# Kernel optimization log

Measured on AMD Instinct MI355X. Metric: run time of the kernel, lower is better.

The kernel has to match this reference:

```python
import jax, jax.numpy as jnp
import numpy as np

B, CIN, COUT, RES, K, WDIM = 16, 512, 512, 64, 3, 512


def setup_inputs() -> dict:
    key = jax.random.key(0)
    ks = jax.random.split(key, 6)
    return {
        "x": jax.random.normal(ks[0], (B, CIN, RES, RES), jnp.float32),
        "w": jax.random.normal(ks[1], (B, WDIM), jnp.float32),
        "affine_w": jax.random.normal(ks[2], (3 * CIN, WDIM), jnp.float32),
        "affine_b": jnp.ones((3 * CIN,), jnp.float32),  # bias_init=1
        "weight": jax.random.normal(ks[3], (COUT, CIN, K, K), jnp.float32),
        "bias": jnp.zeros((COUT,), jnp.float32),
        "noise_const": jax.random.normal(ks[4], (RES, RES), jnp.float32),
        "noise_strength": jnp.zeros((), jnp.float32),
    }


def reference(x, w, affine_w, affine_b, weight, bias, noise_const, noise_strength):
    b, cin, h, wd = x.shape
    cout, _, kh, kw = weight.shape
    wdim = affine_w.shape[1]
    # StyleSplit: FullyConnectedLayer (weight_gain = 1/sqrt(w_dim)) -> chunk3 -> m1*m2+m3
    proj = w @ (affine_w * (1.0 / np.sqrt(wdim))).T + affine_b  # [B, 3*Cin]
    m1, m2, m3 = jnp.split(proj, 3, axis=1)
    styles = m1 * m2 + m3  # [B, Cin]
    # modulate + demodulate (fused_modconv path)
    ww = weight[None] * styles[:, None, :, None, None]  # [B, Cout, Cin, kh, kw]
    dcoefs = jax.lax.rsqrt(jnp.sum(ww * ww, axis=(2, 3, 4)) + 1e-8)  # [B, Cout]
    ww = ww * dcoefs[:, :, None, None, None]
    # batch-as-groups conv (flip_weight=True -> plain cross-correlation), padding = k//2
    pad = kh // 2
    xg = x.reshape(1, b * cin, h, wd)
    wg = ww.reshape(b * cout, cin, kh, kw)
    y = jax.lax.conv_general_dilated(
        xg, wg, window_strides=(1, 1), padding=((pad, pad), (pad, pad)),
        dimension_numbers=("NCHW", "OIHW", "NCHW"), feature_group_count=b)
    y = y.reshape(b, cout, h, wd)
    # const noise
    y = y + noise_const * noise_strength
    # bias_act: lrelu(slope 0.2) with def_gain sqrt(2), gain=1, no clamp
    y = jax.nn.leaky_relu(y + bias[None, :, None, None], 0.2) * np.sqrt(2.0).astype(np.float32)
    return y
```

## Files before the change

kernel.cpp:

```cpp
#include <hip/hip_runtime.h>


#define NCI  512
#define NCO  512

typedef __attribute__((ext_vector_type(8))) short short8;
typedef __attribute__((ext_vector_type(4))) float f32x4;

#define GLDS16(g, l) __builtin_amdgcn_global_load_lds( \
    (const __attribute__((address_space(1))) void*)(g), \
    (__attribute__((address_space(3))) void*)(l), 16, 0, 0)

static __device__ __forceinline__ unsigned short f2bf(float f) {
  unsigned int u = __float_as_uint(f);
  u += 0x7fffu + ((u >> 16) & 1u);
  return (unsigned short)(u >> 16);
}

__global__ __launch_bounds__(256) void k_styles(
    const float* __restrict__ w, const float* __restrict__ aw,
    const float* __restrict__ ab, float* __restrict__ styles) {
  const int ci0 = blockIdx.x * 32, b = blockIdx.y;
  __shared__ float ws[512];
  __shared__ float pm[3][32];
  const int t = threadIdx.x;
  ws[t] = w[b * 512 + t];
  ws[t + 256] = w[b * 512 + 256 + t];
  __syncthreads();
  const int r = t >> 3, k = t & 7;
#pragma unroll
  for (int pass = 0; pass < 3; ++pass) {
    const float* row = aw + (size_t)(ci0 + r + pass * 512) * 512;
    float a = 0.f;
#pragma unroll 4
    for (int i = 0; i < 16; ++i) {
      float4 v = *(const float4*)(row + i * 32 + k * 4);
      float4 u = *(const float4*)(&ws[i * 32 + k * 4]);
      a += v.x * u.x + v.y * u.y + v.z * u.z + v.w * u.w;
    }
    a += __shfl_xor(a, 1); a += __shfl_xor(a, 2); a += __shfl_xor(a, 4);
    if (k == 0) pm[pass][r] = a;
  }
  __syncthreads();
  if (t < 32) {
    const float g = 0.04419417382415922f;
    int j = ci0 + t;
    float m1 = pm[0][t] * g + ab[j];
    float m2 = pm[1][t] * g + ab[j + 512];
    float m3 = pm[2][t] * g + ab[j + 1024];
    styles[b * 512 + j] = m1 * m2 + m3;
  }
}

__global__ __launch_bounds__(256) void k_wt(
    const float* __restrict__ wgt, short* __restrict__ wb2, float* __restrict__ wsq) {
  const int t = blockIdx.x * 256 + threadIdx.x;
  const int co = t >> 9, ci = t & 511;
  const float* p = wgt + (size_t)t * 9;
  const int ci_blk = ci >> 5, co_blk = co >> 6, m = (co >> 4) & 3;
  const int lane2 = ((ci >> 3) & 3) * 16 + (co & 15), e = ci & 7;
  const size_t base = (size_t)(ci_blk * 8 + co_blk) * 18432 + (size_t)m * 512 + lane2 * 8 + e;
  float s = 0.f;
#pragma unroll
  for (int kk = 0; kk < 9; ++kk) {
    float v = p[kk];
    s += v * v;
    wb2[base + (size_t)kk * 2048] = (short)f2bf(v);
  }
  wsq[t] = s;
}

__global__ __launch_bounds__(256) void k_dcoef(
    const float* __restrict__ wsq, const float* __restrict__ styles,
    float* __restrict__ dcoef) {
  const int co0 = blockIdx.x * 32, b = blockIdx.y;
  __shared__ float ss[512];
  const int t = threadIdx.x;
  float s0 = styles[b * 512 + t], s1 = styles[b * 512 + 256 + t];
  ss[t] = s0 * s0;
  ss[t + 256] = s1 * s1;
  __syncthreads();
  const int r = t >> 3, k = t & 7;
  const float* row = wsq + (size_t)(co0 + r) * 512;
  float a = 0.f;
#pragma unroll 4
  for (int i = 0; i < 16; ++i) {
    float4 v = *(const float4*)(row + i * 32 + k * 4);
    float4 u = *(const float4*)(&ss[i * 32 + k * 4]);
    a += v.x * u.x + v.y * u.y + v.z * u.z + v.w * u.w;
  }
  a += __shfl_xor(a, 1); a += __shfl_xor(a, 2); a += __shfl_xor(a, 4);
  if (k == 0) dcoef[b * 512 + co0 + r] = 1.0f / sqrtf(a + 1e-8f);
}

__global__ __launch_bounds__(256) void k_xt(
    const float* __restrict__ x, const float* __restrict__ styles,
    short* __restrict__ xt) {
  const int px0 = blockIdx.x * 64, ci0 = blockIdx.y * 32, b = blockIdx.z;
  __shared__ float tile[32][68];
  const int t = threadIdx.x;
  {
    const int cil = t >> 4, pxq = t & 15;
#pragma unroll
    for (int half = 0; half < 2; ++half) {
      const int c = cil + half * 16;
      float4 v = *(const float4*)(x + ((size_t)(b * 512 + ci0 + c)) * 4096 + px0 + pxq * 4);
      float sc = styles[b * 512 + ci0 + c];
      v.x *= sc; v.y *= sc; v.z *= sc; v.w *= sc;
      *(float4*)(&tile[c][pxq * 4]) = v;
    }
  }
  __syncthreads();
  {
    const int pxl = t >> 2, cig = t & 3;
    short8 o;
#pragma unroll
    for (int e = 0; e < 8; ++e) o[e] = (short)f2bf(tile[cig * 8 + e][pxl]);
    *(short8*)(xt + ((size_t)(b * 4096 + px0 + pxl)) * 512 + ci0 + cig * 8) = o;
  }
}

__global__ __launch_bounds__(256, 2) void k_conv(
    const short* __restrict__ xt, const short* __restrict__ wb2,
    const float* __restrict__ dcoef, const float* __restrict__ bias,
    const float* __restrict__ noise, const float* __restrict__ nstr,
    float* __restrict__ out) {
  const int bid = blockIdx.x;
  const int logical = (bid & 7) * 256 + (bid >> 3);
  const int co0 = (logical & 7) * 64;
  const int h0  = ((logical >> 3) & 15) * 4;
  const int b   = logical >> 7;

  __shared__ short xs2[6][4][66][8];
  __shared__ short wls2[9][4][64][8];
  const int t = threadIdx.x;
  const int lane = t & 63, wave = t >> 6;
  const int lrow = lane & 15, lq = lane >> 4;

  const short8 z8 = {0, 0, 0, 0, 0, 0, 0, 0};
  if (t < 48) {
    int r = t / 8, pc = t & 7;
    *(short8*)(&xs2[r][pc >> 1][(pc & 1) ? 65 : 0][0]) = z8;
  }
  if (h0 == 0)
    for (int i = t; i < 264; i += 256) ((short8*)&xs2[0][0][0][0])[i] = z8;
  if (h0 == 60)
    for (int i = t; i < 264; i += 256) ((short8*)&xs2[5][0][0][0])[i] = z8;

  f32x4 acc[4][4];
#pragma unroll
  for (int m = 0; m < 4; ++m)
#pragma unroll
    for (int n = 0; n < 4; ++n)
#pragma unroll
      for (int e = 0; e < 4; ++e) acc[m][n][e] = 0.f;

  const size_t xb = (size_t)b * 4096 * 512;
  const int cob = co0 >> 6;

  for (int cb = 0; cb < 16; ++cb) {
    const int ci0 = cb * 32;
#pragma unroll
    for (int i = 0; i < 6; ++i) {
      int rp = i * 4 + wave;
      int r = rp >> 2, p = rp & 3;
      int row = h0 - 1 + r;
      if ((unsigned)row < 64u) {
        const short* g = xt + xb + ((size_t)(row * 64 + lane)) * 512 + ci0 + p * 8;
        GLDS16(g, &xs2[r][p][1][0]);
      }
    }
    const short* wbase = wb2 + (size_t)(cb * 8 + cob) * 18432;
#pragma unroll
    for (int i = 0; i < 9; ++i) {
      int c = i * 4 + wave;
      GLDS16(wbase + c * 512 + lane * 8, ((short*)wls2) + c * 512);
    }
    __syncthreads();

#pragma unroll
    for (int kh = 0; kh < 3; ++kh) {
#pragma unroll
      for (int kw = 0; kw < 3; ++kw) {
        const int kk = kh * 3 + kw;
        short8 af[4], bf[4];
#pragma unroll
        for (int m = 0; m < 4; ++m)
          af[m] = *(const short8*)(&wls2[kk][m][lane][0]);
#pragma unroll
        for (int n = 0; n < 4; ++n)
          bf[n] = *(const short8*)(&xs2[wave + kh][lq][n * 16 + lrow + kw][0]);
#pragma unroll
        for (int m = 0; m < 4; ++m)
#pragma unroll
          for (int n = 0; n < 4; ++n)
            acc[m][n] = __builtin_amdgcn_mfma_f32_16x16x32_bf16(af[m], bf[n], acc[m][n], 0, 0, 0);
      }
    }
    __syncthreads();
  }

  const float ns = nstr[0];
  const int h = h0 + wave;
  float dc[4][4], bv[4][4];
#pragma unroll
  for (int m = 0; m < 4; ++m)
#pragma unroll
    for (int r = 0; r < 4; ++r) {
      int co = co0 + m * 16 + lq * 4 + r;
      dc[m][r] = dcoef[b * NCO + co];
      bv[m][r] = bias[co];
    }
#pragma unroll
  for (int n = 0; n < 4; ++n) {
    int wcol = n * 16 + lrow;
    float nz = noise[h * 64 + wcol] * ns;
#pragma unroll
    for (int m = 0; m < 4; ++m) {
#pragma unroll
      for (int r = 0; r < 4; ++r) {
        int co = co0 + m * 16 + lq * 4 + r;
        float v = acc[m][n][r] * dc[m][r] + nz + bv[m][r];
        v = (v > 0.f ? v : 0.2f * v) * 1.4142135623730951f;
        out[(((size_t)b * NCO + co) * 64 + h) * 64 + wcol] = v;
      }
    }
  }
}

extern "C" void kernel_launch(void* const* d_in, const int* in_sizes, int n_in,
                              void* d_out, int out_size, void* d_ws, size_t ws_size,
                              hipStream_t stream) {
  const float* x    = (const float*)d_in[0];
  const float* w    = (const float*)d_in[1];
  const float* aw   = (const float*)d_in[2];
  const float* ab   = (const float*)d_in[3];
  const float* wgt  = (const float*)d_in[4];
  const float* bias = (const float*)d_in[5];
  const float* nc   = (const float*)d_in[6];
  const float* ns   = (const float*)d_in[7];
  float* out = (float*)d_out;

  char* ws = (char*)d_ws;
  float* styles = (float*)(ws);
  float* dcoef  = (float*)(ws + 32768);
  float* wsq    = (float*)(ws + 65536);
  short* wb2    = (short*)(ws + 1114112);
  short* xt     = (short*)(ws + 5832704);

  k_styles<<<dim3(16, 16), dim3(256), 0, stream>>>(w, aw, ab, styles);
  k_wt<<<dim3(1024), dim3(256), 0, stream>>>(wgt, wb2, wsq);
  k_dcoef<<<dim3(16, 16), dim3(256), 0, stream>>>(wsq, styles, dcoef);
  k_xt<<<dim3(64, 16, 16), dim3(256), 0, stream>>>(x, styles, xt);
  k_conv<<<dim3(2048), dim3(256), 0, stream>>>(xt, wb2, dcoef, bias, nc, ns, out);
}
```

Before: 505.9 us.

## Enlarge conv tile to 8 rows per block, swizzle xt LDS, stage weight repack

The conv kernel now gives each block 8 output rows instead of 4, so each wave computes two rows with a 4x8 MFMA accumulator tile. The weight tile loaded from global memory is reused over twice as many pixels, and the grid is halved. Each output channel block is pinned to one XCD for L2 locality. The xt transpose kernel XOR-swizzles its LDS tile to avoid bank conflicts, and the weight repack kernel builds each tile in LDS and writes it out with coalesced 16-byte stores. The larger accumulator raises register pressure and could hurt occupancy under launch_bounds(256,2).

```diff
diff --git a/kernel.cpp b/kernel.cpp
--- a/kernel.cpp
+++ b/kernel.cpp
@@ -54,20 +54,30 @@
 
 __global__ __launch_bounds__(256) void k_wt(
     const float* __restrict__ wgt, short* __restrict__ wb2, float* __restrict__ wsq) {
-  const int t = blockIdx.x * 256 + threadIdx.x;
-  const int co = t >> 9, ci = t & 511;
-  const float* p = wgt + (size_t)t * 9;
-  const int ci_blk = ci >> 5, co_blk = co >> 6, m = (co >> 4) & 3;
-  const int lane2 = ((ci >> 3) & 3) * 16 + (co & 15), e = ci & 7;
-  const size_t base = (size_t)(ci_blk * 8 + co_blk) * 18432 + (size_t)m * 512 + lane2 * 8 + e;
-  float s = 0.f;
-#pragma unroll
-  for (int kk = 0; kk < 9; ++kk) {
-    float v = p[kk];
-    s += v * v;
-    wb2[base + (size_t)kk * 2048] = (short)f2bf(v);
-  }
-  wsq[t] = s;
+  const int co_blk = blockIdx.x & 7, ci_blk = blockIdx.x >> 3;
+  __shared__ short wtile[18432];
+  const int t = threadIdx.x;
+#pragma unroll
+  for (int i = 0; i < 8; ++i) {
+    int idx = i * 256 + t;
+    int co_l = idx >> 5, ci_l = idx & 31;
+    int co = co_blk * 64 + co_l, ci = ci_blk * 32 + ci_l;
+    const float* p = wgt + ((size_t)co * 512 + ci) * 9;
+    int base = (co_l >> 4) * 512 + (((ci_l >> 3) & 3) * 16 + (co_l & 15)) * 8 + (ci_l & 7);
+    float s = 0.f;
+#pragma unroll
+    for (int kk = 0; kk < 9; ++kk) {
+      float v = p[kk];
+      s += v * v;
+      wtile[kk * 2048 + base] = (short)f2bf(v);
+    }
+    wsq[(size_t)co * 512 + ci] = s;
+  }
+  __syncthreads();
+  short8* dst = (short8*)(wb2 + (size_t)(ci_blk * 8 + co_blk) * 18432);
+  const short8* src = (const short8*)wtile;
+#pragma unroll
+  for (int j = 0; j < 9; ++j) dst[j * 256 + t] = src[j * 256 + t];
 }
 
 __global__ __launch_bounds__(256) void k_dcoef(
@@ -107,7 +117,7 @@
       float4 v = *(const float4*)(x + ((size_t)(b * 512 + ci0 + c)) * 4096 + px0 + pxq * 4);
       float sc = styles[b * 512 + ci0 + c];
       v.x *= sc; v.y *= sc; v.z *= sc; v.w *= sc;
-      *(float4*)(&tile[c][pxq * 4]) = v;
+      *(float4*)(&tile[c][4 * (pxq ^ (c & 15))]) = v;
     }
   }
   __syncthreads();
@@ -115,7 +125,10 @@
     const int pxl = t >> 2, cig = t & 3;
     short8 o;
 #pragma unroll
-    for (int e = 0; e < 8; ++e) o[e] = (short)f2bf(tile[cig * 8 + e][pxl]);
+    for (int e = 0; e < 8; ++e) {
+      int R = cig * 8 + e;
+      o[e] = (short)f2bf(tile[R][4 * ((pxl >> 2) ^ (R & 15)) + (pxl & 3)]);
+    }
     *(short8*)(xt + ((size_t)(b * 4096 + px0 + pxl)) * 512 + ci0 + cig * 8) = o;
   }
 }
@@ -126,55 +139,56 @@
     const float* __restrict__ noise, const float* __restrict__ nstr,
     float* __restrict__ out) {
   const int bid = blockIdx.x;
-  const int logical = (bid & 7) * 256 + (bid >> 3);
-  const int co0 = (logical & 7) * 64;
-  const int h0  = ((logical >> 3) & 15) * 4;
-  const int b   = logical >> 7;
-
-  __shared__ short xs2[6][4][66][8];
-  __shared__ short wls2[9][4][64][8];
+  const int xcd = bid & 7, i = bid >> 3;
+  const int co0 = xcd * 64;
+  const int b = i >> 3;
+  const int h0 = (i & 7) * 8;
+
+  __shared__ short xs[10][4][66][8];
+  __shared__ short wls[9][4][64][8];
   const int t = threadIdx.x;
   const int lane = t & 63, wave = t >> 6;
   const int lrow = lane & 15, lq = lane >> 4;
 
   const short8 z8 = {0, 0, 0, 0, 0, 0, 0, 0};
-  if (t < 48) {
+  if (t < 80) {
     int r = t / 8, pc = t & 7;
-    *(short8*)(&xs2[r][pc >> 1][(pc & 1) ? 65 : 0][0]) = z8;
-  }
-  if (h0 == 0)
-    for (int i = t; i < 264; i += 256) ((short8*)&xs2[0][0][0][0])[i] = z8;
-  if (h0 == 60)
-    for (int i = t; i < 264; i += 256) ((short8*)&xs2[5][0][0][0])[i] = z8;
-
-  f32x4 acc[4][4];
+    *(short8*)(&xs[r][pc >> 1][(pc & 1) ? 65 : 0][0]) = z8;
+  }
+  if (h0 == 0) {
+    for (int i2 = t; i2 < 264; i2 += 256) ((short8*)&xs[0][0][0][0])[i2] = z8;
+  }
+  if (h0 == 56) {
+    for (int i2 = t; i2 < 264; i2 += 256) ((short8*)&xs[9][0][0][0])[i2] = z8;
+  }
+
+  f32x4 acc[4][8];
 #pragma unroll
   for (int m = 0; m < 4; ++m)
 #pragma unroll
-    for (int n = 0; n < 4; ++n)
+    for (int n = 0; n < 8; ++n)
 #pragma unroll
       for (int e = 0; e < 4; ++e) acc[m][n][e] = 0.f;
 
   const size_t xb = (size_t)b * 4096 * 512;
-  const int cob = co0 >> 6;
 
   for (int cb = 0; cb < 16; ++cb) {
     const int ci0 = cb * 32;
 #pragma unroll
-    for (int i = 0; i < 6; ++i) {
-      int rp = i * 4 + wave;
+    for (int i2 = 0; i2 < 10; ++i2) {
+      int rp = i2 * 4 + wave;
       int r = rp >> 2, p = rp & 3;
       int row = h0 - 1 + r;
       if ((unsigned)row < 64u) {
         const short* g = xt + xb + ((size_t)(row * 64 + lane)) * 512 + ci0 + p * 8;
-        GLDS16(g, &xs2[r][p][1][0]);
+        GLDS16(g, &xs[r][p][1][0]);
       }
     }
-    const short* wbase = wb2 + (size_t)(cb * 8 + cob) * 18432;
-#pragma unroll
-    for (int i = 0; i < 9; ++i) {
-      int c = i * 4 + wave;
-      GLDS16(wbase + c * 512 + lane * 8, ((short*)wls2) + c * 512);
+    const short* wbase = wb2 + (size_t)(cb * 8 + xcd) * 18432;
+#pragma unroll
+    for (int i2 = 0; i2 < 9; ++i2) {
+      int c = i2 * 4 + wave;
+      GLDS16(wbase + c * 512 + lane * 8, ((short*)wls) + c * 512);
     }
     __syncthreads();
 
@@ -183,17 +197,17 @@
 #pragma unroll
       for (int kw = 0; kw < 3; ++kw) {
         const int kk = kh * 3 + kw;
-        short8 af[4], bf[4];
+        short8 af[4], bf[8];
 #pragma unroll
         for (int m = 0; m < 4; ++m)
-          af[m] = *(const short8*)(&wls2[kk][m][lane][0]);
-#pragma unroll
-        for (int n = 0; n < 4; ++n)
-          bf[n] = *(const short8*)(&xs2[wave + kh][lq][n * 16 + lrow + kw][0]);
+          af[m] = *(const short8*)(&wls[kk][m][lane][0]);
+#pragma unroll
+        for (int n = 0; n < 8; ++n)
+          bf[n] = *(const short8*)(&xs[2 * wave + kh + (n >> 2)][lq][(n & 3) * 16 + lrow + kw][0]);
 #pragma unroll
         for (int m = 0; m < 4; ++m)
 #pragma unroll
-          for (int n = 0; n < 4; ++n)
+          for (int n = 0; n < 8; ++n)
             acc[m][n] = __builtin_amdgcn_mfma_f32_16x16x32_bf16(af[m], bf[n], acc[m][n], 0, 0, 0);
       }
     }
@@ -201,7 +215,6 @@
   }
 
   const float ns = nstr[0];
-  const int h = h0 + wave;
   float dc[4][4], bv[4][4];
 #pragma unroll
   for (int m = 0; m < 4; ++m)
@@ -212,8 +225,9 @@
       bv[m][r] = bias[co];
     }
 #pragma unroll
-  for (int n = 0; n < 4; ++n) {
-    int wcol = n * 16 + lrow;
+  for (int n = 0; n < 8; ++n) {
+    int h = h0 + 2 * wave + (n >> 2);
+    int wcol = (n & 3) * 16 + lrow;
     float nz = noise[h * 64 + wcol] * ns;
 #pragma unroll
     for (int m = 0; m < 4; ++m) {
@@ -249,8 +263,8 @@
   short* xt     = (short*)(ws + 5832704);
 
   k_styles<<<dim3(16, 16), dim3(256), 0, stream>>>(w, aw, ab, styles);
-  k_wt<<<dim3(1024), dim3(256), 0, stream>>>(wgt, wb2, wsq);
+  k_wt<<<dim3(128), dim3(256), 0, stream>>>(wgt, wb2, wsq);
   k_dcoef<<<dim3(16, 16), dim3(256), 0, stream>>>(wsq, styles, dcoef);
   k_xt<<<dim3(64, 16, 16), dim3(256), 0, stream>>>(x, styles, xt);
-  k_conv<<<dim3(2048), dim3(256), 0, stream>>>(xt, wb2, dcoef, bias, nc, ns, out);
-}
+  k_conv<<<dim3(1024), dim3(256), 0, stream>>>(xt, wb2, dcoef, bias, nc, ns, out);
+}
```

Measured after the change: 493.1 us. -2.5%, faster.
